# Performance work log

Hardware: AMD Instinct MI355X
Metric: run time of the kernel (lower is better)

The kernel has to match this reference:

```python
import jax, jax.numpy as jnp
import numpy as np

N = 100000
IN_DIM = 128
OUT_DIM = 128
E = 3200000


def setup_inputs() -> dict:
    key = jax.random.key(0)
    k1, k2, k3, k4, k5 = jax.random.split(key, 5)
    x = jax.random.normal(k1, (N, IN_DIM), dtype=jnp.float32)
    src = jax.random.randint(k2, (E,), 0, N)
    dst = jax.random.randint(k3, (E,), 0, N)
    edge_index = jnp.stack([src, dst], axis=0)  # (2, E) int
    # Linear(2*in_dim, out_dim): torch stores weight as (out, in)
    bound = 1.0 / np.sqrt(2 * IN_DIM)
    W = jax.random.uniform(k4, (OUT_DIM, 2 * IN_DIM), minval=-bound, maxval=bound, dtype=jnp.float32)
    b = jax.random.uniform(k5, (OUT_DIM,), minval=-bound, maxval=bound, dtype=jnp.float32)
    return {"x": x, "edge_index": edge_index, "W": W, "b": b}


def reference(x, edge_index, W, b):
    # x: (N, d), edge_index: (2, E)
    n = x.shape[0]
    src, dst = edge_index[0], edge_index[1]
    # scatter-add of source features into target buckets (mean aggregation)
    agg = jax.ops.segment_sum(x[src], dst, num_segments=n)          # (N, d)
    count = jax.ops.segment_sum(jnp.ones((src.shape[0],), x.dtype), dst, num_segments=n)
    count = jnp.maximum(count, 1.0)[:, None]                         # (N, 1)
    neigh_mean = agg / count
    combined = jnp.concatenate([x, neigh_mean], axis=1)              # (N, 2d)
    return combined @ W.T + b
```

## Files before the change

### kernel.cpp

```cpp
#include <hip/hip_runtime.h>

typedef unsigned int u32;
typedef unsigned short u16;
typedef unsigned char u8;
typedef __bf16 bf16x8 __attribute__((ext_vector_type(8)));
typedef float f32x4 __attribute__((ext_vector_type(4)));
typedef float f32x2 __attribute__((ext_vector_type(2)));

__device__ __forceinline__ u16 f2bf(float f) {
  u32 u = __builtin_bit_cast(u32, f);
  u32 r = (u + 0x7fffu + ((u >> 16) & 1u)) >> 16;
  return (u16)r;
}

__global__ __launch_bounds__(256) void pre_k(const float* __restrict__ x, u16* __restrict__ xbf,
                                             u32* __restrict__ xq,
                                             const float* __restrict__ W, u16* __restrict__ wbf,
                                             const int* __restrict__ dst, int E,
                                             u32* __restrict__ bktTotal, int N, int nbkt,
                                             int nba, int nbx) {
  int b = blockIdx.x, tid = threadIdx.x;
  if (b < nba) {
    __shared__ u32 h[512];
    for (int t = tid; t < 512; t += 256) h[t] = 0u;
    __syncthreads();
    int base = b * 8192;
    for (int it = 0; it < 32; it++) {
      int i = base + it * 256 + tid;
      if (i < E) atomicAdd(&h[(u32)dst[i] >> 8], 1u);
    }
    __syncthreads();
    for (int t = tid; t < nbkt; t += 256) {
      u32 c = h[t];
      if (c) atomicAdd(&bktTotal[t], c);
    }
  } else if (b < nba + nbx) {
    int i = (b - nba) * 256 + tid;
    if (i < N * 32) {
      const float4 v = *(const float4*)(x + (size_t)i * 4);
      ushort4 o = { f2bf(v.x), f2bf(v.y), f2bf(v.z), f2bf(v.w) };
      *(ushort4*)(xbf + (size_t)i * 4) = o;
      u32 p = 0;
      p = __builtin_amdgcn_cvt_pk_fp8_f32(v.x, v.y, p, false);
      p = __builtin_amdgcn_cvt_pk_fp8_f32(v.z, v.w, p, true);
      xq[i] = p;
    }
  } else {
    int i = (b - nba - nbx) * 256 + tid;
    if (i < 8192) {
      const float4 v = *(const float4*)(W + (size_t)i * 4);
      ushort4 o = { f2bf(v.x), f2bf(v.y), f2bf(v.z), f2bf(v.w) };
      *(ushort4*)(wbf + (size_t)i * 4) = o;
    }
  }
}

__global__ __launch_bounds__(512) void bscan_k(const u32* __restrict__ bktTotal, int nbkt,
                                               int E, int N, u32* __restrict__ start,
                                               u32* __restrict__ cursor, u32* __restrict__ offsets) {
  __shared__ u32 s[512];
  int t = threadIdx.x;
  u32 v = (t < nbkt) ? bktTotal[t] : 0u;
  s[t] = v;
  __syncthreads();
  for (int off = 1; off < 512; off <<= 1) {
    u32 x = (t >= off) ? s[t - off] : 0u;
    __syncthreads();
    s[t] += x;
    __syncthreads();
  }
  u32 excl = s[t] - v;
  if (t < nbkt) { start[t] = excl; cursor[t] = excl; }
  if (t == nbkt - 1) start[nbkt] = excl + v;
  if (t == 0) offsets[N] = (u32)E;
}

__global__ __launch_bounds__(256) void part_k(const int* __restrict__ src, const int* __restrict__ dst,
                                              int E, u32* __restrict__ cursor,
                                              u32* __restrict__ packed, int nbkt) {
  __shared__ u32 h[512];
  for (int t = threadIdx.x; t < 512; t += 256) h[t] = 0u;
  __syncthreads();
  int base = blockIdx.x * 8192;
  for (int it = 0; it < 32; it++) {
    int i = base + it * 256 + threadIdx.x;
    if (i < E) atomicAdd(&h[(u32)dst[i] >> 8], 1u);
  }
  __syncthreads();
  for (int t = threadIdx.x; t < nbkt; t += 256) {
    u32 c = h[t];
    h[t] = c ? atomicAdd(&cursor[t], c) : 0u;
  }
  __syncthreads();
  for (int it = 0; it < 32; it++) {
    int i = base + it * 256 + threadIdx.x;
    if (i < E) {
      u32 d = (u32)dst[i];
      u32 pos = atomicAdd(&h[d >> 8], 1u);
      packed[pos] = (u32)src[i] | ((d & 255u) << 24);
    }
  }
}

__global__ __launch_bounds__(256) void bucket_k(const u32* __restrict__ packed,
                                                const u32* __restrict__ start, int N,
                                                u32* __restrict__ offsets, int* __restrict__ ssrc,
                                                u8* __restrict__ nodeperm) {
  __shared__ u32 cnt[256];
  __shared__ u32 scn[256];
  __shared__ u32 cur[256];
  int b = blockIdx.x, t = threadIdx.x;
  u32 lo = start[b], hi = start[b + 1];
  cnt[t] = 0u;
  __syncthreads();
  for (u32 j = lo + t; j < hi; j += 256) atomicAdd(&cnt[packed[j] >> 24], 1u);
  __syncthreads();
  u32 v = cnt[t];
  scn[t] = v;
  __syncthreads();
  for (int off = 1; off < 256; off <<= 1) {
    u32 x = (t >= off) ? scn[t - off] : 0u;
    __syncthreads();
    scn[t] += x;
    __syncthreads();
  }
  u32 base = lo + scn[t] - v;
  int node = b * 256 + t;
  if (node < N) offsets[node] = base;
  cur[t] = base;
  __syncthreads();
  for (u32 j = lo + t; j < hi; j += 256) {
    u32 w = packed[j];
    u32 pos = atomicAdd(&cur[w >> 24], 1u);
    ssrc[pos] = (int)(w & 0xFFFFFFu);
  }
  {
    int g = t >> 6, l = t & 63;
    u32 mykey = cnt[t] * 256u + (u32)l;
    const u32* cg = &cnt[g * 64];
    u32 rank = 0;
#pragma unroll 8
    for (int l2 = 0; l2 < 64; l2++) {
      u32 k2 = cg[l2] * 256u + (u32)l2;
      rank += (k2 < mykey) ? 1u : 0u;
    }
    nodeperm[(size_t)b * 256 + g * 64 + rank] = (u8)l;
  }
}

#define DECX(vv) { f32x2 p;                                                    \
    p = __builtin_amdgcn_cvt_pk_f32_fp8((vv).x, false); acc[0] += p;           \
    p = __builtin_amdgcn_cvt_pk_f32_fp8((vv).x, true);  acc[1] += p;           \
    p = __builtin_amdgcn_cvt_pk_f32_fp8((vv).y, false); acc[2] += p;           \
    p = __builtin_amdgcn_cvt_pk_f32_fp8((vv).y, true);  acc[3] += p;           \
    p = __builtin_amdgcn_cvt_pk_f32_fp8((vv).z, false); acc[4] += p;           \
    p = __builtin_amdgcn_cvt_pk_f32_fp8((vv).z, true);  acc[5] += p;           \
    p = __builtin_amdgcn_cvt_pk_f32_fp8((vv).w, false); acc[6] += p;           \
    p = __builtin_amdgcn_cvt_pk_f32_fp8((vv).w, true);  acc[7] += p; }

#define ROWS4(R0, R1, R2, R3, I) {                                             \
    R0 = *(const uint4*)(xqb + ((size_t)(I).x << 7) + lofs);                   \
    R1 = *(const uint4*)(xqb + ((size_t)(I).y << 7) + lofs);                   \
    R2 = *(const uint4*)(xqb + ((size_t)(I).z << 7) + lofs);                   \
    R3 = *(const uint4*)(xqb + ((size_t)(I).w << 7) + lofs); }

__global__ __launch_bounds__(256) void fuse_k(const int* __restrict__ ssrc,
                                              const u32* __restrict__ offsets,
                                              const u32* __restrict__ xq,
                                              const u16* __restrict__ xbf,
                                              const u16* __restrict__ wbf,
                                              const float* __restrict__ bias,
                                              const u8* __restrict__ nodeperm,
                                              float* __restrict__ out, int N) {
  __shared__ u16 mlds[64][136];
  int wv = threadIdx.x >> 6, lane = threadIdx.x & 63;
  int sub = lane >> 3, c8 = lane & 7;
  int nbase = blockIdx.x * 64;
  const char* xqb = (const char*)xq;
  const int lofs = c8 << 4;

  for (int r = 0; r < 2; r++) {
    int ln = nodeperm[(size_t)nbase + r * 32 + wv * 8 + sub];
    int node = nbase + ln;
    f32x2 acc[8];
#pragma unroll
    for (int i = 0; i < 8; i++) acc[i] = f32x2{0.f, 0.f};
    u32 deg = 0;
    if (node < N) {
      u32 s0 = offsets[node], s1 = offsets[node + 1];
      deg = s1 - s0;
      u32 j = s0;
      u32 nq = deg >> 2;
      u32 npair = nq >> 1;
      if (npair) {
        uint4 iA = *(const uint4*)(ssrc + j);
        uint4 iB = *(const uint4*)(ssrc + j + 4);
        uint4 a0, a1, a2, a3, b0, b1, b2, b3;
        ROWS4(a0, a1, a2, a3, iA)
        for (u32 p = 1; p < npair; p++) {
          ROWS4(b0, b1, b2, b3, iB)
          iA = *(const uint4*)(ssrc + j + 8);
          iB = *(const uint4*)(ssrc + j + 12);
          DECX(a0) DECX(a1) DECX(a2) DECX(a3)
          ROWS4(a0, a1, a2, a3, iA)
          DECX(b0) DECX(b1) DECX(b2) DECX(b3)
          j += 8;
        }
        ROWS4(b0, b1, b2, b3, iB)
        DECX(a0) DECX(a1) DECX(a2) DECX(a3)
        DECX(b0) DECX(b1) DECX(b2) DECX(b3)
        j += 8;
      }
      if (nq & 1) {
        uint4 iT = *(const uint4*)(ssrc + j);
        uint4 t0, t1, t2, t3;
        ROWS4(t0, t1, t2, t3, iT)
        DECX(t0) DECX(t1) DECX(t2) DECX(t3)
        j += 4;
      }
      for (; j < s1; j++) {
        int e = ssrc[j];
        uint4 v = *(const uint4*)(xqb + ((size_t)e << 7) + lofs);
        DECX(v)
      }
    }
    float inv = 1.0f / (float)(deg ? deg : 1u);
    u32 o[8];
#pragma unroll
    for (int k = 0; k < 8; k++)
      o[k] = (u32)f2bf(acc[k].x * inv) | ((u32)f2bf(acc[k].y * inv) << 16);
    u32* mp = (u32*)&mlds[ln][c8 * 16];
    *(uint4*)(mp + 0) = uint4{o[0], o[1], o[2], o[3]};
    *(uint4*)(mp + 4) = uint4{o[4], o[5], o[6], o[7]};
  }
  __syncthreads();

  int la = lane & 15, lb = lane >> 4;
  int wbase = nbase + wv * 16;
  bf16x8 a[8];
  const u16* ab = xbf + ((size_t)(wbase + la) << 7) + lb * 8;
#pragma unroll
  for (int kb = 0; kb < 4; kb++) a[kb] = *(const bf16x8*)(ab + kb * 32);
#pragma unroll
  for (int kb = 0; kb < 4; kb++) a[4 + kb] = *(const bf16x8*)(&mlds[wv * 16 + la][kb * 32 + lb * 8]);

#pragma unroll
  for (int ct = 0; ct < 8; ct++) {
    f32x4 accr = { 0.f, 0.f, 0.f, 0.f };
    const u16* bbase = wbf + ((size_t)(ct * 16 + la) << 8) + lb * 8;
#pragma unroll
    for (int kb = 0; kb < 8; kb++) {
      bf16x8 b = *(const bf16x8*)(bbase + kb * 32);
      accr = __builtin_amdgcn_mfma_f32_16x16x32_bf16(a[kb], b, accr, 0, 0, 0);
    }
    float bc = bias[ct * 16 + la];
#pragma unroll
    for (int jj = 0; jj < 4; jj++) {
      int rr = wbase + lb * 4 + jj;
      if (rr < N) out[((size_t)rr << 7) + ct * 16 + la] = accr[jj] + bc;
    }
  }
}

extern "C" void kernel_launch(void* const* d_in, const int* in_sizes, int n_in,
                              void* d_out, int out_size, void* d_ws, size_t ws_size,
                              hipStream_t stream) {
  const float* x    = (const float*)d_in[0];
  const int*   ei   = (const int*)d_in[1];
  const float* W    = (const float*)d_in[2];
  const float* bias = (const float*)d_in[3];
  const int N = in_sizes[0] / 128;
  const int E = in_sizes[1] / 2;
  const int nbkt = (N + 255) >> 8;
  const int* src = ei;
  const int* dst = ei + E;
  float* out = (float*)d_out;

  u32* packed   = (u32*)d_out;
  u32* bktTotal = packed + E;
  u32* start    = bktTotal + nbkt;
  u32* cursor   = start + nbkt + 1;

  char* ws = (char*)d_ws;
  u32* offsets = (u32*)ws;
  size_t off = ((size_t)(N + 1) * 4 + 255) & ~(size_t)255;
  int* ssrc = (int*)(ws + off);
  off += (size_t)E * 4;
  off = (off + 255) & ~(size_t)255;
  u16* xbf = (u16*)(ws + off);
  off += (size_t)N * 128 * 2;
  off = (off + 255) & ~(size_t)255;
  u32* xq = (u32*)(ws + off);
  off += (size_t)N * 128;
  off = (off + 255) & ~(size_t)255;
  u16* wbf = (u16*)(ws + off);
  off += (size_t)128 * 256 * 2;
  off = (off + 255) & ~(size_t)255;
  u8* nodeperm = (u8*)(ws + off);

  const int nbx = (N * 32 + 255) / 256;
  const int nba = (E + 8191) / 8192;
  hipMemsetAsync(bktTotal, 0, (size_t)nbkt * 4, stream);
  pre_k<<<nba + nbx + 32, 256, 0, stream>>>(x, xbf, xq, W, wbf, dst, E, bktTotal, N, nbkt, nba, nbx);
  bscan_k<<<1, 512, 0, stream>>>(bktTotal, nbkt, E, N, start, cursor, offsets);
  part_k<<<nba, 256, 0, stream>>>(src, dst, E, cursor, packed, nbkt);
  bucket_k<<<nbkt, 256, 0, stream>>>(packed, start, N, offsets, ssrc, nodeperm);
  fuse_k<<<(N + 63) / 64, 256, 0, stream>>>(ssrc, offsets, xq, xbf, wbf, bias, nodeperm, out, N);
}
```

Measured before the change: 217.0 us.

## Stream edge-batched gathers via async global-to-LDS loads with segmented node reduction

Replaces the per-node gather loop (8 lanes per node, nodes sorted by degree via nodeperm) with a wave-wide flat stream over the contiguous edge range of its 16 nodes. Each 32-edge chunk's source indices are broadcast with ds_bpermute, and the fp8 rows are fetched with global_load_lds into double-buffered LDS staging behind explicit vmcnt waits. Node boundaries are handled by masked accumulation plus a shuffle reduction when a node closes. This removes the degree-imbalance stalls and the nodeperm ranking work, at the cost of more LDS, per-batch boundary branches and cross-lane reductions.

```diff
diff --git a/kernel.cpp b/kernel.cpp
--- a/kernel.cpp
+++ b/kernel.cpp
@@ -104,8 +104,7 @@
 
 __global__ __launch_bounds__(256) void bucket_k(const u32* __restrict__ packed,
                                                 const u32* __restrict__ start, int N,
-                                                u32* __restrict__ offsets, int* __restrict__ ssrc,
-                                                u8* __restrict__ nodeperm) {
+                                                u32* __restrict__ offsets, int* __restrict__ ssrc) {
   __shared__ u32 cnt[256];
   __shared__ u32 scn[256];
   __shared__ u32 cur[256];
@@ -134,35 +133,92 @@
     u32 pos = atomicAdd(&cur[w >> 24], 1u);
     ssrc[pos] = (int)(w & 0xFFFFFFu);
   }
-  {
-    int g = t >> 6, l = t & 63;
-    u32 mykey = cnt[t] * 256u + (u32)l;
-    const u32* cg = &cnt[g * 64];
-    u32 rank = 0;
-#pragma unroll 8
-    for (int l2 = 0; l2 < 64; l2++) {
-      u32 k2 = cg[l2] * 256u + (u32)l2;
-      rank += (k2 < mykey) ? 1u : 0u;
-    }
-    nodeperm[(size_t)b * 256 + g * 64 + rank] = (u8)l;
-  }
-}
-
-#define DECX(vv) { f32x2 p;                                                    \
-    p = __builtin_amdgcn_cvt_pk_f32_fp8((vv).x, false); acc[0] += p;           \
-    p = __builtin_amdgcn_cvt_pk_f32_fp8((vv).x, true);  acc[1] += p;           \
-    p = __builtin_amdgcn_cvt_pk_f32_fp8((vv).y, false); acc[2] += p;           \
-    p = __builtin_amdgcn_cvt_pk_f32_fp8((vv).y, true);  acc[3] += p;           \
-    p = __builtin_amdgcn_cvt_pk_f32_fp8((vv).z, false); acc[4] += p;           \
-    p = __builtin_amdgcn_cvt_pk_f32_fp8((vv).z, true);  acc[5] += p;           \
-    p = __builtin_amdgcn_cvt_pk_f32_fp8((vv).w, false); acc[6] += p;           \
-    p = __builtin_amdgcn_cvt_pk_f32_fp8((vv).w, true);  acc[7] += p; }
-
-#define ROWS4(R0, R1, R2, R3, I) {                                             \
-    R0 = *(const uint4*)(xqb + ((size_t)(I).x << 7) + lofs);                   \
-    R1 = *(const uint4*)(xqb + ((size_t)(I).y << 7) + lofs);                   \
-    R2 = *(const uint4*)(xqb + ((size_t)(I).z << 7) + lofs);                   \
-    R3 = *(const uint4*)(xqb + ((size_t)(I).w << 7) + lofs); }
+}
+
+
+#define DECP(W) { f32x2 q_; \
+  q_ = __builtin_amdgcn_cvt_pk_f32_fp8((W).x, false); acc[0] += q_; \
+  q_ = __builtin_amdgcn_cvt_pk_f32_fp8((W).x, true);  acc[1] += q_; \
+  q_ = __builtin_amdgcn_cvt_pk_f32_fp8((W).y, false); acc[2] += q_; \
+  q_ = __builtin_amdgcn_cvt_pk_f32_fp8((W).y, true);  acc[3] += q_; \
+  q_ = __builtin_amdgcn_cvt_pk_f32_fp8((W).z, false); acc[4] += q_; \
+  q_ = __builtin_amdgcn_cvt_pk_f32_fp8((W).z, true);  acc[5] += q_; \
+  q_ = __builtin_amdgcn_cvt_pk_f32_fp8((W).w, false); acc[6] += q_; \
+  q_ = __builtin_amdgcn_cvt_pk_f32_fp8((W).w, true);  acc[7] += q_; }
+
+__device__ __forceinline__ void close_node(f32x2* acc, u32 deg, int lrow, int lane,
+                                           u16 (*mlds)[136]) {
+#pragma unroll
+  for (int m = 1; m <= 4; m <<= 1) {
+#pragma unroll
+    for (int i = 0; i < 8; i++) {
+      acc[i].x += __shfl_xor(acc[i].x, m);
+      acc[i].y += __shfl_xor(acc[i].y, m);
+    }
+  }
+  float inv = 1.0f / (float)(deg ? deg : 1u);
+  if ((lane & 7) == 0) {
+    int s8 = lane >> 3;
+    u32 o[8];
+#pragma unroll
+    for (int k = 0; k < 8; k++)
+      o[k] = (u32)f2bf(acc[k].x * inv) | ((u32)f2bf(acc[k].y * inv) << 16);
+    u32* mp = (u32*)&mlds[lrow][s8 * 16];
+    *(uint4*)(mp + 0) = uint4{o[0], o[1], o[2], o[3]};
+    *(uint4*)(mp + 4) = uint4{o[4], o[5], o[6], o[7]};
+  }
+#pragma unroll
+  for (int i = 0; i < 8; i++) acc[i] = f32x2{0.f, 0.f};
+}
+
+__device__ __forceinline__ void consume_batch(uint4 w, u32 p, int lane, f32x2* acc,
+                                              u32& s0node, u32& s1c, int& cnode, int nlast,
+                                              int nbaseblk, const u32* __restrict__ offsets,
+                                              u16 (*mlds)[136]) {
+  u32 pos = p + (u32)(lane & 7);
+  u32 pend = p + 8u;
+  for (;;) {
+    if (cnode > nlast) break;
+    if (s1c >= pend) {
+      if (s0node <= p) { DECP(w) }
+      else {
+        bool in = pos >= s0node;
+        uint4 wm = { in ? w.x : 0u, in ? w.y : 0u, in ? w.z : 0u, in ? w.w : 0u };
+        DECP(wm)
+      }
+      break;
+    }
+    {
+      bool in = (pos >= s0node) && (pos < s1c);
+      uint4 wm = { in ? w.x : 0u, in ? w.y : 0u, in ? w.z : 0u, in ? w.w : 0u };
+      DECP(wm)
+    }
+    close_node(acc, s1c - s0node, cnode - nbaseblk, lane, mlds);
+    cnode++;
+    s0node = s1c;
+    if (cnode <= nlast) s1c = offsets[cnode + 1];
+  }
+}
+
+#define ILOAD(CB) { u32 jj = (CB) + (u32)(lane & 31); if (jj > Em1) jj = Em1; \
+                    vidx = (u32)ssrc[jj]; }
+
+#define BPERM() { int pb = (lane & 7) * 4; \
+    bp0 = __builtin_amdgcn_ds_bpermute(pb,      (int)vidx); \
+    bp1 = __builtin_amdgcn_ds_bpermute(pb + 32, (int)vidx); \
+    bp2 = __builtin_amdgcn_ds_bpermute(pb + 64, (int)vidx); \
+    bp3 = __builtin_amdgcn_ds_bpermute(pb + 96, (int)vidx); }
+
+#define GISS(PAR, B, BP) { \
+    const char* gsrc = xqb + (((size_t)(u32)(BP)) << 7) + ((lane >> 3) << 4); \
+    __builtin_amdgcn_global_load_lds((const u32*)gsrc, \
+        (u32*)(stg + ((PAR) * 4 + (B)) * 1024), 16, 0, 0); }
+
+#define CONS(PAR, B, IMM, CB) { \
+    asm volatile("s_waitcnt vmcnt(" #IMM ")" ::: "memory"); \
+    uint4 w = *(const uint4*)(stg + ((PAR) * 4 + (B)) * 1024 + (lane << 4)); \
+    consume_batch(w, (CB) + (B) * 8u, lane, acc, s0node, s1c, cnode, nlast, \
+                  nbaseblk, offsets, mlds); }
 
 __global__ __launch_bounds__(256) void fuse_k(const int* __restrict__ ssrc,
                                               const u32* __restrict__ offsets,
@@ -170,94 +226,80 @@
                                               const u16* __restrict__ xbf,
                                               const u16* __restrict__ wbf,
                                               const float* __restrict__ bias,
-                                              const u8* __restrict__ nodeperm,
-                                              float* __restrict__ out, int N) {
+                                              float* __restrict__ out, int N, int E) {
+  __shared__ u8 stg_all[4][8192];
   __shared__ u16 mlds[64][136];
   int wv = threadIdx.x >> 6, lane = threadIdx.x & 63;
-  int sub = lane >> 3, c8 = lane & 7;
-  int nbase = blockIdx.x * 64;
+  int nbaseblk = blockIdx.x * 64;
+  int wbase = nbaseblk + wv * 16;
   const char* xqb = (const char*)xq;
-  const int lofs = c8 << 4;
-
-  for (int r = 0; r < 2; r++) {
-    int ln = nodeperm[(size_t)nbase + r * 32 + wv * 8 + sub];
-    int node = nbase + ln;
+  u8* stg = stg_all[wv];
+
+  if (wbase < N) {
+    int nlast = wbase + 15; if (nlast > N - 1) nlast = N - 1;
+    u32 S0 = offsets[wbase];
+    u32 S1 = offsets[nlast + 1];
+    u32 Em1 = (u32)E - 1u;
+    int nc = (int)((S1 - S0 + 31u) >> 5);
+
+    int cnode = wbase;
+    u32 s0node = S0;
+    u32 s1c = offsets[wbase + 1];
     f32x2 acc[8];
 #pragma unroll
     for (int i = 0; i < 8; i++) acc[i] = f32x2{0.f, 0.f};
-    u32 deg = 0;
-    if (node < N) {
-      u32 s0 = offsets[node], s1 = offsets[node + 1];
-      deg = s1 - s0;
-      u32 j = s0;
-      u32 nq = deg >> 2;
-      u32 npair = nq >> 1;
-      if (npair) {
-        uint4 iA = *(const uint4*)(ssrc + j);
-        uint4 iB = *(const uint4*)(ssrc + j + 4);
-        uint4 a0, a1, a2, a3, b0, b1, b2, b3;
-        ROWS4(a0, a1, a2, a3, iA)
-        for (u32 p = 1; p < npair; p++) {
-          ROWS4(b0, b1, b2, b3, iB)
-          iA = *(const uint4*)(ssrc + j + 8);
-          iB = *(const uint4*)(ssrc + j + 12);
-          DECX(a0) DECX(a1) DECX(a2) DECX(a3)
-          ROWS4(a0, a1, a2, a3, iA)
-          DECX(b0) DECX(b1) DECX(b2) DECX(b3)
-          j += 8;
-        }
-        ROWS4(b0, b1, b2, b3, iB)
-        DECX(a0) DECX(a1) DECX(a2) DECX(a3)
-        DECX(b0) DECX(b1) DECX(b2) DECX(b3)
-        j += 8;
-      }
-      if (nq & 1) {
-        uint4 iT = *(const uint4*)(ssrc + j);
-        uint4 t0, t1, t2, t3;
-        ROWS4(t0, t1, t2, t3, iT)
-        DECX(t0) DECX(t1) DECX(t2) DECX(t3)
-        j += 4;
-      }
-      for (; j < s1; j++) {
-        int e = ssrc[j];
-        uint4 v = *(const uint4*)(xqb + ((size_t)e << 7) + lofs);
-        DECX(v)
-      }
-    }
-    float inv = 1.0f / (float)(deg ? deg : 1u);
-    u32 o[8];
-#pragma unroll
-    for (int k = 0; k < 8; k++)
-      o[k] = (u32)f2bf(acc[k].x * inv) | ((u32)f2bf(acc[k].y * inv) << 16);
-    u32* mp = (u32*)&mlds[ln][c8 * 16];
-    *(uint4*)(mp + 0) = uint4{o[0], o[1], o[2], o[3]};
-    *(uint4*)(mp + 4) = uint4{o[4], o[5], o[6], o[7]};
-  }
-  __syncthreads();
-
-  int la = lane & 15, lb = lane >> 4;
-  int wbase = nbase + wv * 16;
-  bf16x8 a[8];
-  const u16* ab = xbf + ((size_t)(wbase + la) << 7) + lb * 8;
-#pragma unroll
-  for (int kb = 0; kb < 4; kb++) a[kb] = *(const bf16x8*)(ab + kb * 32);
-#pragma unroll
-  for (int kb = 0; kb < 4; kb++) a[4 + kb] = *(const bf16x8*)(&mlds[wv * 16 + la][kb * 32 + lb * 8]);
-
-#pragma unroll
-  for (int ct = 0; ct < 8; ct++) {
-    f32x4 accr = { 0.f, 0.f, 0.f, 0.f };
-    const u16* bbase = wbf + ((size_t)(ct * 16 + la) << 8) + lb * 8;
-#pragma unroll
-    for (int kb = 0; kb < 8; kb++) {
-      bf16x8 b = *(const bf16x8*)(bbase + kb * 32);
-      accr = __builtin_amdgcn_mfma_f32_16x16x32_bf16(a[kb], b, accr, 0, 0, 0);
-    }
-    float bc = bias[ct * 16 + la];
-#pragma unroll
-    for (int jj = 0; jj < 4; jj++) {
-      int rr = wbase + lb * 4 + jj;
-      if (rr < N) out[((size_t)rr << 7) + ct * 16 + la] = accr[jj] + bc;
+
+    if (nc > 0) {
+      u32 vidx; int bp0, bp1, bp2, bp3;
+      ILOAD(S0)
+      BPERM()
+      ILOAD(S0 + 32u)
+      GISS(0, 0, bp0) GISS(0, 1, bp1) GISS(0, 2, bp2) GISS(0, 3, bp3)
+      for (int c = 0; c < nc - 1; c++) {
+        int par = c & 1, npar = par ^ 1;
+        BPERM()
+        ILOAD(S0 + ((u32)c + 2u) * 32u)
+        GISS(npar, 0, bp0) GISS(npar, 1, bp1) GISS(npar, 2, bp2) GISS(npar, 3, bp3)
+        u32 cb = S0 + (u32)c * 32u;
+        CONS(par, 0, 8, cb) CONS(par, 1, 7, cb) CONS(par, 2, 6, cb) CONS(par, 3, 5, cb)
+      }
+      {
+        int par = (nc - 1) & 1;
+        u32 cb = S0 + ((u32)nc - 1u) * 32u;
+        CONS(par, 0, 3, cb) CONS(par, 1, 2, cb) CONS(par, 2, 1, cb) CONS(par, 3, 0, cb)
+      }
+    }
+    while (cnode <= nlast) {
+      close_node(acc, s1c - s0node, cnode - nbaseblk, lane, mlds);
+      cnode++;
+      s0node = s1c;
+      if (cnode <= nlast) s1c = offsets[cnode + 1];
+    }
+
+    int la = lane & 15, lb = lane >> 4;
+    bf16x8 a[8];
+    const u16* ab = xbf + ((size_t)(wbase + la) << 7) + lb * 8;
+#pragma unroll
+    for (int kb = 0; kb < 4; kb++) a[kb] = *(const bf16x8*)(ab + kb * 32);
+#pragma unroll
+    for (int kb = 0; kb < 4; kb++)
+      a[4 + kb] = *(const bf16x8*)(&mlds[wv * 16 + la][kb * 32 + lb * 8]);
+
+#pragma unroll
+    for (int ct = 0; ct < 8; ct++) {
+      f32x4 accr = { 0.f, 0.f, 0.f, 0.f };
+      const u16* bbase = wbf + ((size_t)(ct * 16 + la) << 8) + lb * 8;
+#pragma unroll
+      for (int kb = 0; kb < 8; kb++) {
+        bf16x8 bv = *(const bf16x8*)(bbase + kb * 32);
+        accr = __builtin_amdgcn_mfma_f32_16x16x32_bf16(a[kb], bv, accr, 0, 0, 0);
+      }
+      float bc = bias[ct * 16 + la];
+#pragma unroll
+      for (int jj = 0; jj < 4; jj++) {
+        int rr = wbase + lb * 4 + jj;
+        if (rr < N) out[((size_t)rr << 7) + ct * 16 + la] = accr[jj] + bc;
+      }
     }
   }
 }
@@ -294,9 +336,6 @@
   off += (size_t)N * 128;
   off = (off + 255) & ~(size_t)255;
   u16* wbf = (u16*)(ws + off);
-  off += (size_t)128 * 256 * 2;
-  off = (off + 255) & ~(size_t)255;
-  u8* nodeperm = (u8*)(ws + off);
 
   const int nbx = (N * 32 + 255) / 256;
   const int nba = (E + 8191) / 8192;
@@ -304,6 +343,6 @@
   pre_k<<<nba + nbx + 32, 256, 0, stream>>>(x, xbf, xq, W, wbf, dst, E, bktTotal, N, nbkt, nba, nbx);
   bscan_k<<<1, 512, 0, stream>>>(bktTotal, nbkt, E, N, start, cursor, offsets);
   part_k<<<nba, 256, 0, stream>>>(src, dst, E, cursor, packed, nbkt);
-  bucket_k<<<nbkt, 256, 0, stream>>>(packed, start, N, offsets, ssrc, nodeperm);
-  fuse_k<<<(N + 63) / 64, 256, 0, stream>>>(ssrc, offsets, xq, xbf, wbf, bias, nodeperm, out, N);
-}
+  bucket_k<<<nbkt, 256, 0, stream>>>(packed, start, N, offsets, ssrc);
+  fuse_k<<<(N + 63) / 64, 256, 0, stream>>>(ssrc, offsets, xq, xbf, wbf, bias, out, N, E);
+}
```

New measurement: 269.7 us. 24.3% more time.

## Gather fp16 rows with packed-half accumulation instead of fp8 gather

Applied to the files above, without the earlier changes.

Drops the separate fp8 copy of x. The neighbour gather now reads the fp16 copy that also feeds the matmul, and accumulates with packed half adds instead of converting fp8 to fp32 and adding in fp32. Blocks shrink to 32 nodes with 16 lanes per node, the node-permutation groups are resized to match, and the MFMA switches to f16 with waves splitting the output columns. This removes a conversion pass and the extra pre-kernel write, and cuts ALU work in the gather, but doubles gather bytes and accumulates in fp16, so precision and overflow become a risk at high degree.

```diff
diff --git a/kernel.cpp b/kernel.cpp
--- a/kernel.cpp
+++ b/kernel.cpp
@@ -3,9 +3,9 @@
 typedef unsigned int u32;
 typedef unsigned short u16;
 typedef unsigned char u8;
-typedef __bf16 bf16x8 __attribute__((ext_vector_type(8)));
+typedef _Float16 half8 __attribute__((ext_vector_type(8)));
+typedef _Float16 h2 __attribute__((ext_vector_type(2)));
 typedef float f32x4 __attribute__((ext_vector_type(4)));
-typedef float f32x2 __attribute__((ext_vector_type(2)));
 
 __device__ __forceinline__ u16 f2bf(float f) {
   u32 u = __builtin_bit_cast(u32, f);
@@ -13,9 +13,8 @@
   return (u16)r;
 }
 
-__global__ __launch_bounds__(256) void pre_k(const float* __restrict__ x, u16* __restrict__ xbf,
-                                             u32* __restrict__ xq,
-                                             const float* __restrict__ W, u16* __restrict__ wbf,
+__global__ __launch_bounds__(256) void pre_k(const float* __restrict__ x, u16* __restrict__ xh,
+                                             const float* __restrict__ W, u16* __restrict__ wh,
                                              const int* __restrict__ dst, int E,
                                              u32* __restrict__ bktTotal, int N, int nbkt,
                                              int nba, int nbx) {
@@ -38,19 +37,17 @@
     int i = (b - nba) * 256 + tid;
     if (i < N * 32) {
       const float4 v = *(const float4*)(x + (size_t)i * 4);
-      ushort4 o = { f2bf(v.x), f2bf(v.y), f2bf(v.z), f2bf(v.w) };
-      *(ushort4*)(xbf + (size_t)i * 4) = o;
-      u32 p = 0;
-      p = __builtin_amdgcn_cvt_pk_fp8_f32(v.x, v.y, p, false);
-      p = __builtin_amdgcn_cvt_pk_fp8_f32(v.z, v.w, p, true);
-      xq[i] = p;
+      u32 p0 = __builtin_bit_cast(u32, __builtin_amdgcn_cvt_pkrtz(v.x, v.y));
+      u32 p1 = __builtin_bit_cast(u32, __builtin_amdgcn_cvt_pkrtz(v.z, v.w));
+      *(uint2*)(xh + (size_t)i * 4) = uint2{p0, p1};
     }
   } else {
     int i = (b - nba - nbx) * 256 + tid;
     if (i < 8192) {
       const float4 v = *(const float4*)(W + (size_t)i * 4);
-      ushort4 o = { f2bf(v.x), f2bf(v.y), f2bf(v.z), f2bf(v.w) };
-      *(ushort4*)(wbf + (size_t)i * 4) = o;
+      u32 p0 = __builtin_bit_cast(u32, __builtin_amdgcn_cvt_pkrtz(v.x, v.y));
+      u32 p1 = __builtin_bit_cast(u32, __builtin_amdgcn_cvt_pkrtz(v.z, v.w));
+      *(uint2*)(wh + (size_t)i * 4) = uint2{p0, p1};
     }
   }
 }
@@ -135,129 +132,107 @@
     ssrc[pos] = (int)(w & 0xFFFFFFu);
   }
   {
-    int g = t >> 6, l = t & 63;
+    int g = t >> 5, l = t & 31;
     u32 mykey = cnt[t] * 256u + (u32)l;
-    const u32* cg = &cnt[g * 64];
+    const u32* cg = &cnt[g * 32];
     u32 rank = 0;
 #pragma unroll 8
-    for (int l2 = 0; l2 < 64; l2++) {
+    for (int l2 = 0; l2 < 32; l2++) {
       u32 k2 = cg[l2] * 256u + (u32)l2;
       rank += (k2 < mykey) ? 1u : 0u;
     }
-    nodeperm[(size_t)b * 256 + g * 64 + rank] = (u8)l;
-  }
-}
-
-#define DECX(vv) { f32x2 p;                                                    \
-    p = __builtin_amdgcn_cvt_pk_f32_fp8((vv).x, false); acc[0] += p;           \
-    p = __builtin_amdgcn_cvt_pk_f32_fp8((vv).x, true);  acc[1] += p;           \
-    p = __builtin_amdgcn_cvt_pk_f32_fp8((vv).y, false); acc[2] += p;           \
-    p = __builtin_amdgcn_cvt_pk_f32_fp8((vv).y, true);  acc[3] += p;           \
-    p = __builtin_amdgcn_cvt_pk_f32_fp8((vv).z, false); acc[4] += p;           \
-    p = __builtin_amdgcn_cvt_pk_f32_fp8((vv).z, true);  acc[5] += p;           \
-    p = __builtin_amdgcn_cvt_pk_f32_fp8((vv).w, false); acc[6] += p;           \
-    p = __builtin_amdgcn_cvt_pk_f32_fp8((vv).w, true);  acc[7] += p; }
-
-#define ROWS4(R0, R1, R2, R3, I) {                                             \
-    R0 = *(const uint4*)(xqb + ((size_t)(I).x << 7) + lofs);                   \
-    R1 = *(const uint4*)(xqb + ((size_t)(I).y << 7) + lofs);                   \
-    R2 = *(const uint4*)(xqb + ((size_t)(I).z << 7) + lofs);                   \
-    R3 = *(const uint4*)(xqb + ((size_t)(I).w << 7) + lofs); }
+    nodeperm[(size_t)b * 256 + g * 32 + rank] = (u8)l;
+  }
+}
+
+#define ACC4(V) { a0 += __builtin_bit_cast(h2, (V).x); a1 += __builtin_bit_cast(h2, (V).y); \
+                  a2 += __builtin_bit_cast(h2, (V).z); a3 += __builtin_bit_cast(h2, (V).w); }
 
 __global__ __launch_bounds__(256) void fuse_k(const int* __restrict__ ssrc,
                                               const u32* __restrict__ offsets,
-                                              const u32* __restrict__ xq,
-                                              const u16* __restrict__ xbf,
-                                              const u16* __restrict__ wbf,
+                                              const u16* __restrict__ xh,
+                                              const u16* __restrict__ wh,
                                               const float* __restrict__ bias,
                                               const u8* __restrict__ nodeperm,
                                               float* __restrict__ out, int N) {
-  __shared__ u16 mlds[64][136];
+  __shared__ u16 mlds[32][136];
   int wv = threadIdx.x >> 6, lane = threadIdx.x & 63;
-  int sub = lane >> 3, c8 = lane & 7;
-  int nbase = blockIdx.x * 64;
-  const char* xqb = (const char*)xq;
-  const int lofs = c8 << 4;
+  int sub = lane >> 4, cl = lane & 15;
+  int nbase = blockIdx.x * 32;
+  const char* xhb = (const char*)xh;
+  const int lofs = cl << 4;
 
   for (int r = 0; r < 2; r++) {
-    int ln = nodeperm[(size_t)nbase + r * 32 + wv * 8 + sub];
+    int ln = nodeperm[(size_t)nbase + r * 16 + wv * 4 + sub];
     int node = nbase + ln;
-    f32x2 acc[8];
-#pragma unroll
-    for (int i = 0; i < 8; i++) acc[i] = f32x2{0.f, 0.f};
+    h2 a0{0,0}, a1{0,0}, a2{0,0}, a3{0,0};
     u32 deg = 0;
     if (node < N) {
       u32 s0 = offsets[node], s1 = offsets[node + 1];
       deg = s1 - s0;
       u32 j = s0;
       u32 nq = deg >> 2;
-      u32 npair = nq >> 1;
-      if (npair) {
+      if (nq) {
         uint4 iA = *(const uint4*)(ssrc + j);
-        uint4 iB = *(const uint4*)(ssrc + j + 4);
-        uint4 a0, a1, a2, a3, b0, b1, b2, b3;
-        ROWS4(a0, a1, a2, a3, iA)
-        for (u32 p = 1; p < npair; p++) {
-          ROWS4(b0, b1, b2, b3, iB)
-          iA = *(const uint4*)(ssrc + j + 8);
-          iB = *(const uint4*)(ssrc + j + 12);
-          DECX(a0) DECX(a1) DECX(a2) DECX(a3)
-          ROWS4(a0, a1, a2, a3, iA)
-          DECX(b0) DECX(b1) DECX(b2) DECX(b3)
-          j += 8;
+        for (u32 q = 1; q < nq; q++) {
+          uint4 iN = *(const uint4*)(ssrc + j + 4);
+          uint4 v0 = *(const uint4*)(xhb + ((size_t)iA.x << 8) + lofs);
+          uint4 v1 = *(const uint4*)(xhb + ((size_t)iA.y << 8) + lofs);
+          uint4 v2 = *(const uint4*)(xhb + ((size_t)iA.z << 8) + lofs);
+          uint4 v3 = *(const uint4*)(xhb + ((size_t)iA.w << 8) + lofs);
+          ACC4(v0) ACC4(v1) ACC4(v2) ACC4(v3)
+          iA = iN; j += 4;
         }
-        ROWS4(b0, b1, b2, b3, iB)
-        DECX(a0) DECX(a1) DECX(a2) DECX(a3)
-        DECX(b0) DECX(b1) DECX(b2) DECX(b3)
-        j += 8;
-      }
-      if (nq & 1) {
-        uint4 iT = *(const uint4*)(ssrc + j);
-        uint4 t0, t1, t2, t3;
-        ROWS4(t0, t1, t2, t3, iT)
-        DECX(t0) DECX(t1) DECX(t2) DECX(t3)
-        j += 4;
+        {
+          uint4 v0 = *(const uint4*)(xhb + ((size_t)iA.x << 8) + lofs);
+          uint4 v1 = *(const uint4*)(xhb + ((size_t)iA.y << 8) + lofs);
+          uint4 v2 = *(const uint4*)(xhb + ((size_t)iA.z << 8) + lofs);
+          uint4 v3 = *(const uint4*)(xhb + ((size_t)iA.w << 8) + lofs);
+          ACC4(v0) ACC4(v1) ACC4(v2) ACC4(v3)
+          j += 4;
+        }
       }
       for (; j < s1; j++) {
         int e = ssrc[j];
-        uint4 v = *(const uint4*)(xqb + ((size_t)e << 7) + lofs);
-        DECX(v)
+        uint4 v = *(const uint4*)(xhb + ((size_t)e << 8) + lofs);
+        ACC4(v)
       }
     }
-    float inv = 1.0f / (float)(deg ? deg : 1u);
-    u32 o[8];
-#pragma unroll
-    for (int k = 0; k < 8; k++)
-      o[k] = (u32)f2bf(acc[k].x * inv) | ((u32)f2bf(acc[k].y * inv) << 16);
-    u32* mp = (u32*)&mlds[ln][c8 * 16];
-    *(uint4*)(mp + 0) = uint4{o[0], o[1], o[2], o[3]};
-    *(uint4*)(mp + 4) = uint4{o[4], o[5], o[6], o[7]};
+    _Float16 ih = (_Float16)(1.0f / (float)(deg ? deg : 1u));
+    h2 iv{ih, ih};
+    h2 m0 = a0 * iv, m1 = a1 * iv, m2 = a2 * iv, m3 = a3 * iv;
+    uint4 o{__builtin_bit_cast(u32, m0), __builtin_bit_cast(u32, m1),
+            __builtin_bit_cast(u32, m2), __builtin_bit_cast(u32, m3)};
+    *(uint4*)&mlds[ln][cl * 8] = o;
   }
   __syncthreads();
 
   int la = lane & 15, lb = lane >> 4;
-  int wbase = nbase + wv * 16;
-  bf16x8 a[8];
-  const u16* ab = xbf + ((size_t)(wbase + la) << 7) + lb * 8;
-#pragma unroll
-  for (int kb = 0; kb < 4; kb++) a[kb] = *(const bf16x8*)(ab + kb * 32);
-#pragma unroll
-  for (int kb = 0; kb < 4; kb++) a[4 + kb] = *(const bf16x8*)(&mlds[wv * 16 + la][kb * 32 + lb * 8]);
-
-#pragma unroll
-  for (int ct = 0; ct < 8; ct++) {
-    f32x4 accr = { 0.f, 0.f, 0.f, 0.f };
-    const u16* bbase = wbf + ((size_t)(ct * 16 + la) << 8) + lb * 8;
+  int strip = wv & 1, ch = wv >> 1;
+  int rbase = nbase + strip * 16;
+  half8 a[8];
+  const u16* ab = xh + ((size_t)(rbase + la) << 7) + lb * 8;
+#pragma unroll
+  for (int kb = 0; kb < 4; kb++) a[kb] = *(const half8*)(ab + kb * 32);
+#pragma unroll
+  for (int kb = 0; kb < 4; kb++)
+    a[4 + kb] = *(const half8*)(&mlds[strip * 16 + la][kb * 32 + lb * 8]);
+
+#pragma unroll
+  for (int c = 0; c < 4; c++) {
+    int ct = ch * 4 + c;
+    f32x4 acc = { 0.f, 0.f, 0.f, 0.f };
+    const u16* bbase = wh + ((size_t)(ct * 16 + la) << 8) + lb * 8;
 #pragma unroll
     for (int kb = 0; kb < 8; kb++) {
-      bf16x8 b = *(const bf16x8*)(bbase + kb * 32);
-      accr = __builtin_amdgcn_mfma_f32_16x16x32_bf16(a[kb], b, accr, 0, 0, 0);
+      half8 b = *(const half8*)(bbase + kb * 32);
+      acc = __builtin_amdgcn_mfma_f32_16x16x32_f16(a[kb], b, acc, 0, 0, 0);
     }
     float bc = bias[ct * 16 + la];
 #pragma unroll
     for (int jj = 0; jj < 4; jj++) {
-      int rr = wbase + lb * 4 + jj;
-      if (rr < N) out[((size_t)rr << 7) + ct * 16 + la] = accr[jj] + bc;
+      int rr = rbase + lb * 4 + jj;
+      if (rr < N) out[((size_t)rr << 7) + ct * 16 + la] = acc[jj] + bc;
     }
   }
 }
@@ -287,13 +262,10 @@
   int* ssrc = (int*)(ws + off);
   off += (size_t)E * 4;
   off = (off + 255) & ~(size_t)255;
-  u16* xbf = (u16*)(ws + off);
+  u16* xh = (u16*)(ws + off);
   off += (size_t)N * 128 * 2;
   off = (off + 255) & ~(size_t)255;
-  u32* xq = (u32*)(ws + off);
-  off += (size_t)N * 128;
-  off = (off + 255) & ~(size_t)255;
-  u16* wbf = (u16*)(ws + off);
+  u16* wh = (u16*)(ws + off);
   off += (size_t)128 * 256 * 2;
   off = (off + 255) & ~(size_t)255;
   u8* nodeperm = (u8*)(ws + off);
@@ -301,9 +273,9 @@
   const int nbx = (N * 32 + 255) / 256;
   const int nba = (E + 8191) / 8192;
   hipMemsetAsync(bktTotal, 0, (size_t)nbkt * 4, stream);
-  pre_k<<<nba + nbx + 32, 256, 0, stream>>>(x, xbf, xq, W, wbf, dst, E, bktTotal, N, nbkt, nba, nbx);
+  pre_k<<<nba + nbx + 32, 256, 0, stream>>>(x, xh, W, wh, dst, E, bktTotal, N, nbkt, nba, nbx);
   bscan_k<<<1, 512, 0, stream>>>(bktTotal, nbkt, E, N, start, cursor, offsets);
   part_k<<<nba, 256, 0, stream>>>(src, dst, E, cursor, packed, nbkt);
   bucket_k<<<nbkt, 256, 0, stream>>>(packed, start, N, offsets, ssrc, nodeperm);
-  fuse_k<<<(N + 63) / 64, 256, 0, stream>>>(ssrc, offsets, xq, xbf, wbf, bias, nodeperm, out, N);
-}
+  fuse_k<<<(N + 31) / 32, 256, 0, stream>>>(ssrc, offsets, xh, wh, bias, nodeperm, out, N);
+}
```

New measurement: 244.3 us. 1.13x slower.
